# Optimization experiments

Hardware: AMD Instinct MI355X
Metric: run time of the kernel (lower is better)

Reference implementation:

```python
import jax, jax.numpy as jnp
import numpy as np

B, T, H, W, C = 32, 32, 28, 28, 1
F = 48   # conv filters
U = 8    # lstm units
EPS = 1e-3  # keras BatchNormalization default epsilon


def setup_inputs() -> dict:
    key = jax.random.key(0)
    ks = jax.random.split(key, 10)
    s = lambda fan_in: 1.0 / np.sqrt(fan_in)
    return {
        "x": jax.random.normal(ks[0], (B, T, H, W, C), jnp.float32),
        "w1": jax.random.normal(ks[1], (3, 3, C, F), jnp.float32) * s(9 * C),
        "b1": jnp.zeros((F,), jnp.float32),
        "w2": jax.random.normal(ks[2], (3, 3, F, F), jnp.float32) * s(9 * F),
        "b2": jnp.zeros((F,), jnp.float32),
        "w3": jax.random.normal(ks[3], (3, 3, F, F), jnp.float32) * s(9 * F),
        "b3": jnp.zeros((F,), jnp.float32),
        "bn1_g": jnp.ones((F,), jnp.float32),
        "bn1_b": jnp.zeros((F,), jnp.float32),
        "bn1_m": jnp.zeros((F,), jnp.float32),
        "bn1_v": jnp.ones((F,), jnp.float32),
        "wf": jax.random.normal(ks[4], (F + U, U), jnp.float32) * s(F + U),
        "bf": jnp.zeros((U,), jnp.float32),
        "wi1": jax.random.normal(ks[5], (F + U, U), jnp.float32) * s(F + U),
        "bi1": jnp.zeros((U,), jnp.float32),
        "wi2": jax.random.normal(ks[6], (F + U, U), jnp.float32) * s(F + U),
        "bi2": jnp.zeros((U,), jnp.float32),
        "wo": jax.random.normal(ks[7], (F + U, U), jnp.float32) * s(F + U),
        "bo": jnp.zeros((U,), jnp.float32),
        "bn2_g": jnp.ones((U,), jnp.float32),
        "bn2_b": jnp.zeros((U,), jnp.float32),
        "bn2_m": jnp.zeros((U,), jnp.float32),
        "bn2_v": jnp.ones((U,), jnp.float32),
        "w_out": jax.random.normal(ks[8], (U, 1), jnp.float32) * s(U),
        "b_out": jnp.zeros((1,), jnp.float32),
    }


def _conv_relu(x, w, b):
    # x: [N, H, W, Cin], w: [3, 3, Cin, Cout], SAME padding
    y = jax.lax.conv_general_dilated(
        x, w, window_strides=(1, 1), padding="SAME",
        dimension_numbers=("NHWC", "HWIO", "NHWC"))
    return jax.nn.relu(y + b)


def _bn_inf(x, g, b, m, v):
    return (x - m) * jax.lax.rsqrt(v + EPS) * g + b


def _forward(x, w1, b1, w2, b2, w3, b3, bn1_g, bn1_b, bn1_m, bn1_v,
             wf, bf, wi1, bi1, wi2, bi2, wo, bo,
             bn2_g, bn2_b, bn2_m, bn2_v, w_out, b_out):
    Bb, Tt = x.shape[0], x.shape[1]
    xf = x.reshape(Bb * Tt, H, W, C)            # fold time into batch for convs
    xf = _conv_relu(xf, w1, b1)
    xf = _conv_relu(xf, w2, b2)
    xf = _conv_relu(xf, w3, b3)
    xf = _bn_inf(xf, bn1_g, bn1_b, bn1_m, bn1_v)
    feats = xf.mean(axis=(1, 2)).reshape(Bb, Tt, F)   # GlobalAvgPool2D per frame

    def step(carry, xt):
        c, h = carry
        z = jnp.concatenate([xt, h], axis=-1)          # [B, F+U]
        f = jax.nn.sigmoid(z @ wf + bf)
        i = jax.nn.sigmoid(z @ wi1 + bi1)
        g = jnp.tanh(z @ wi2 + bi2)
        o = jax.nn.sigmoid(z @ wo + bo)
        c_new = f * c + i * g
        h_new = o * jnp.tanh(c_new)
        return (c_new, h_new), h_new

    init = (jnp.zeros((Bb, U), x.dtype), jnp.zeros((Bb, U), x.dtype))
    _, hs = jax.lax.scan(step, init, jnp.swapaxes(feats, 0, 1))  # [T, B, U]
    hs = jnp.swapaxes(hs, 0, 1)                                   # [B, T, U]
    y = _bn_inf(hs, bn2_g, bn2_b, bn2_m, bn2_v)
    return y @ w_out + b_out                                      # [B, T, 1]


def reference(x, w1, b1, w2, b2, w3, b3, bn1_g, bn1_b, bn1_m, bn1_v,
              wf, bf, wi1, bi1, wi2, bi2, wo, bo,
              bn2_g, bn2_b, bn2_m, bn2_v, w_out, b_out):
    return _forward(x, w1, b1, w2, b2, w3, b3, bn1_g, bn1_b, bn1_m, bn1_v,
                    wf, bf, wi1, bi1, wi2, bi2, wo, bo,
                    bn2_g, bn2_b, bn2_m, bn2_v, w_out, b_out)
```

## Files before the change

kernel.cpp:

```cpp
#include <hip/hip_runtime.h>
#include <stdint.h>

#define B_ 32
#define T_ 32
#define NPIX 784
#define NFRM 1024
#define EPSV 1e-3f

typedef __attribute__((ext_vector_type(8))) _Float16 half8v;
typedef __attribute__((ext_vector_type(4))) float float4v;

#define CB_STRIDE 12576
#define ZERO_OFF  75456
#define X_OFF     75472
#define W_OFF     78608
#define LDS_TOT   121616
#define WPACK     43008

__device__ __forceinline__ unsigned short f2h(float f) {
    union { _Float16 h; unsigned short u; } cv; cv.h = (_Float16)f; return cv.u;
}

__global__ __launch_bounds__(256) void pack_weights(
    const float* __restrict__ w2, const float* __restrict__ w3,
    unsigned short* __restrict__ out)
{
    int idx = blockIdx.x * 256 + threadIdx.x;
    int conv = idx / 21504;
    int r = idx - conv * 21504;
    const float* w = conv ? w3 : w2;
    int s  = r / 1536;
    int r2 = r - s * 1536;
    int q  = r2 / 384;
    int r3 = r2 - q * 384;
    int co = r3 >> 3, j = r3 & 7;
    int k  = s * 32 + q * 8 + j;
    unsigned short v = 0;
    if (k < 432) v = f2h(w[k * 48 + co]);
    out[idx] = v;
}

__device__ __forceinline__ void stage_w(char* smem, const char* g, int tid) {
    const char* gl = g + tid * 16;
    __builtin_amdgcn_global_load_lds(
        (const __attribute__((address_space(1))) unsigned int*)(gl),
        (__attribute__((address_space(3))) unsigned int*)(smem + W_OFF + tid * 16),
        16, 0, 0);
    __builtin_amdgcn_global_load_lds(
        (const __attribute__((address_space(1))) unsigned int*)(gl + 16384),
        (__attribute__((address_space(3))) unsigned int*)(smem + W_OFF + tid * 16 + 16384),
        16, 0, 0);
    if (tid < 640)
        __builtin_amdgcn_global_load_lds(
            (const __attribute__((address_space(1))) unsigned int*)(gl + 32768),
            (__attribute__((address_space(3))) unsigned int*)(smem + W_OFF + tid * 16 + 32768),
            16, 0, 0);
}

#define KLOOP                                                                  \
    _Pragma("unroll 2")                                                        \
    for (int s = 0; s < 14; ++s) {                                             \
        const char* wb = smem + W_OFF + bB + s * 3072;                         \
        half8v bv0 = *(const half8v*)(wb);                                     \
        half8v bv1 = *(const half8v*)(wb + 256);                               \
        half8v bv2 = *(const half8v*)(wb + 512);                               \
        const int k_   = s * 32 + q * 8;                                       \
        const int tap_ = (k_ * 1366) >> 16;         \
        const int kc_  = k_ - tap_ * 48;                                       \
        const int ty_  = (tap_ * 11) >> 5;            \
        const int tx_  = tap_ - ty_ * 3;                                       \
        const int aoff_ = (kc_ >> 3) * CB_STRIDE + (ty_ * 28 + tx_) * 16;      \
        _Pragma("unroll")                                                      \
        for (int mt = 0; mt < 4; ++mt) {                                       \
            if (mt < 3 || wid == 0) {                                          \
                int ad = pixb16[mt] + aoff_;                                   \
                ad = ((msks[mt] >> s) & 1) ? ad : ZERO_OFF;                    \
                half8v a = *(const half8v*)(smem + ad);                        \
                acc[mt][0] = __builtin_amdgcn_mfma_f32_16x16x32_f16(a, bv0, acc[mt][0], 0, 0, 0); \
                acc[mt][1] = __builtin_amdgcn_mfma_f32_16x16x32_f16(a, bv1, acc[mt][1], 0, 0, 0); \
                acc[mt][2] = __builtin_amdgcn_mfma_f32_16x16x32_f16(a, bv2, acc[mt][2], 0, 0, 0); \
            }                                                                  \
        }                                                                      \
    }

__global__ __launch_bounds__(1024, 1) void fused_cnn(
    const float* __restrict__ x,
    const float* __restrict__ w1, const float* __restrict__ b1,
    const float* __restrict__ b2, const float* __restrict__ b3,
    const unsigned short* __restrict__ wpack,
    float* __restrict__ feats,
    const float* __restrict__ bn_g, const float* __restrict__ bn_b,
    const float* __restrict__ bn_m, const float* __restrict__ bn_v)
{
    __shared__ __align__(16) char smem[LDS_TOT];
    const int tid = threadIdx.x;
    const int n = blockIdx.x;
    const int lane = tid & 63, wid = tid >> 6;
    const int l15 = lane & 15, q = lane >> 4;

    if (tid < 4) *(unsigned int*)(smem + ZERO_OFF + tid * 4) = 0;
    if (tid < NPIX) ((float*)(smem + X_OFF))[tid] = x[(size_t)n * NPIX + tid];
    stage_w(smem, (const char*)wpack, tid);
    __syncthreads();

    if (tid < NPIX) {
        const float* sx = (const float*)(smem + X_OFF);
        int y = tid / 28, xx = tid % 28;
        #pragma unroll
        for (int h = 0; h < 2; ++h) {
            float a[24];
            #pragma unroll
            for (int c = 0; c < 24; ++c) a[c] = b1[h * 24 + c];
            #pragma unroll
            for (int dy = 0; dy < 3; ++dy) {
                int yy = y + dy - 1;
                if ((unsigned)yy >= 28u) continue;
                #pragma unroll
                for (int dx = 0; dx < 3; ++dx) {
                    int xc = xx + dx - 1;
                    if ((unsigned)xc >= 28u) continue;
                    float xv = sx[yy * 28 + xc];
                    const float* wr = w1 + (dy * 3 + dx) * 48 + h * 24;
                    #pragma unroll
                    for (int c = 0; c < 24; ++c) a[c] += xv * wr[c];
                }
            }
            #pragma unroll
            for (int c2 = 0; c2 < 3; ++c2) {
                half8v hv;
                #pragma unroll
                for (int j = 0; j < 8; ++j)
                    hv[j] = (_Float16)fmaxf(a[c2 * 8 + j], 0.f);
                *(half8v*)(smem + (h * 3 + c2) * CB_STRIDE + tid * 16) = hv;
            }
        }
    }
    __syncthreads();

    const int bB = q * 768 + l15 * 16;

    float4v acc[4][3];
    int pixb16[4], msks[4];
    #pragma unroll
    for (int mt = 0; mt < 4; ++mt) {
        int tt = wid + mt * 16;
        int p  = tt * 16 + l15;
        int y  = (p * 9363) >> 18;
        int x2 = p - y * 28;
        pixb16[mt] = (p - 29) * 16;
        unsigned my0 = ((unsigned)(y - 1) < 28u) ? 0x007u : 0u;
        unsigned my1 = ((unsigned)(y    ) < 28u) ? 0x038u : 0u;
        unsigned my2 = ((unsigned)(y + 1) < 28u) ? 0x1C0u : 0u;
        unsigned mx0 = ((unsigned)(x2 - 1) < 28u) ? 0x049u : 0u;
        unsigned mx1 = ((unsigned)(x2    ) < 28u) ? 0x092u : 0u;
        unsigned mx2 = ((unsigned)(x2 + 1) < 28u) ? 0x124u : 0u;
        unsigned m9 = (my0 | my1 | my2) & (mx0 | mx1 | mx2);
        if (tt >= 49) m9 = 0;
        int mm = 0;
        #pragma unroll
        for (int s = 0; s < 14; ++s) {
            int k = s * 32 + q * 8;
            int tap = (k * 1366) >> 16;
            if ((m9 >> tap) & 1) mm |= (1 << s);
        }
        msks[mt] = mm;
        #pragma unroll
        for (int nt = 0; nt < 3; ++nt) {
            float bv = b2[nt * 16 + l15];
            acc[mt][nt] = (float4v){bv, bv, bv, bv};
        }
    }

    KLOOP

    __syncthreads();

    #pragma unroll
    for (int mt = 0; mt < 4; ++mt) {
        int tt = wid + mt * 16;
        if (tt >= 49) continue;
        #pragma unroll
        for (int nt = 0; nt < 3; ++nt) {
            int c = nt * 16 + l15;
            #pragma unroll
            for (int r = 0; r < 4; ++r) {
                int p = tt * 16 + q * 4 + r;
                unsigned int us = (unsigned int)f2h(fmaxf(acc[mt][nt][r], 0.f));
                unsigned int other = __shfl_xor(us, 1);
                if (!(l15 & 1)) {
                    unsigned int dw = us | (other << 16);
                    *(unsigned int*)(smem + (c >> 3) * CB_STRIDE + (c & 7) * 2 + p * 16) = dw;
                }
            }
        }
    }
    stage_w(smem, (const char*)wpack + WPACK, tid);
    __syncthreads();

    #pragma unroll
    for (int mt = 0; mt < 4; ++mt)
        #pragma unroll
        for (int nt = 0; nt < 3; ++nt) {
            float bv = b3[nt * 16 + l15];
            acc[mt][nt] = (float4v){bv, bv, bv, bv};
        }

    KLOOP

    float ps0 = 0.f, ps1 = 0.f, ps2 = 0.f;
    #pragma unroll
    for (int mt = 0; mt < 4; ++mt) {
        int tt = wid + mt * 16;
        if (tt >= 49) continue;
        #pragma unroll
        for (int r = 0; r < 4; ++r) {
            ps0 += fmaxf(acc[mt][0][r], 0.f);
            ps1 += fmaxf(acc[mt][1][r], 0.f);
            ps2 += fmaxf(acc[mt][2][r], 0.f);
        }
    }
    ps0 += __shfl_xor(ps0, 16); ps0 += __shfl_xor(ps0, 32);
    ps1 += __shfl_xor(ps1, 16); ps1 += __shfl_xor(ps1, 32);
    ps2 += __shfl_xor(ps2, 16); ps2 += __shfl_xor(ps2, 32);
    __syncthreads();
    float* sRed = (float*)smem;
    if (lane < 16) {
        sRed[wid * 48 + l15]      = ps0;
        sRed[wid * 48 + 16 + l15] = ps1;
        sRed[wid * 48 + 32 + l15] = ps2;
    }
    __syncthreads();
    if (tid < 48) {
        float s = 0.f;
        #pragma unroll
        for (int wv = 0; wv < 16; ++wv) s += sRed[wv * 48 + tid];
        float r  = rsqrtf(bn_v[tid] + EPSV);
        float sc = r * bn_g[tid] * (1.0f / 784.0f);
        float sh = bn_b[tid] - bn_m[tid] * r * bn_g[tid];
        feats[(size_t)n * 48 + tid] = s * sc + sh;
    }
}

__global__ __launch_bounds__(64) void lstm_kernel(
    const float* __restrict__ feats,
    const float* __restrict__ wf, const float* __restrict__ bfv,
    const float* __restrict__ wi1, const float* __restrict__ bi1,
    const float* __restrict__ wi2, const float* __restrict__ bi2,
    const float* __restrict__ wo, const float* __restrict__ bov,
    const float* __restrict__ g2, const float* __restrict__ b2v,
    const float* __restrict__ m2, const float* __restrict__ v2,
    const float* __restrict__ w_out, const float* __restrict__ b_out,
    float* __restrict__ out)
{
    __shared__ float sZ[56];
    __shared__ float sG[32];
    __shared__ float sS[8];
    __shared__ float sKs;

    int tid = threadIdx.x;
    int b = blockIdx.x;
    int gu = tid & 31, g = gu >> 3, u = gu & 7, half = tid >> 5;

    const float* wsrc = (g == 0) ? wf : (g == 1) ? wi1 : (g == 2) ? wi2 : wo;
    float wreg[28];
    #pragma unroll
    for (int j = 0; j < 28; ++j) wreg[j] = wsrc[(half * 28 + j) * 8 + u];
    float bias = ((g == 0) ? bfv : (g == 1) ? bi1 : (g == 2) ? bi2 : bov)[u];

    if (tid < 8) {
        float r = rsqrtf(v2[tid] + EPSV);
        sS[tid] = r * g2[tid] * w_out[tid];
        sZ[48 + tid] = 0.f;
    }
    if (tid == 0) {
        float k = b_out[0];
        for (int uu = 0; uu < 8; ++uu) {
            float r = rsqrtf(v2[uu] + EPSV);
            k += (b2v[uu] - m2[uu] * r * g2[uu]) * w_out[uu];
        }
        sKs = k;
    }

    float c = 0.f;
    const float* fb = feats + (size_t)b * T_ * 48;

    for (int t = 0; t < T_; ++t) {
        if (tid < 48) sZ[tid] = fb[t * 48 + tid];
        __syncthreads();

        float a = 0.f;
        #pragma unroll
        for (int j = 0; j < 28; ++j) a += sZ[half * 28 + j] * wreg[j];
        a += __shfl_xor(a, 32);
        a += bias;
        float v;
        if (g == 2) { float e = __expf(2.f * a); v = 1.f - 2.f / (e + 1.f); }
        else        { v = 1.f / (1.f + __expf(-a)); }
        if (tid < 32) sG[gu] = v;
        __syncthreads();

        if (tid < 8) {
            c = sG[tid] * c + sG[8 + tid] * sG[16 + tid];
            float e = __expf(2.f * c);
            float h = sG[24 + tid] * (1.f - 2.f / (e + 1.f));
            sZ[48 + tid] = h;
            float contrib = h * sS[tid];
            contrib += __shfl_xor(contrib, 1);
            contrib += __shfl_xor(contrib, 2);
            contrib += __shfl_xor(contrib, 4);
            if (tid == 0) out[b * T_ + t] = contrib + sKs;
        }
        __syncthreads();
    }
}

extern "C" void kernel_launch(void* const* d_in, const int* in_sizes, int n_in,
                              void* d_out, int out_size, void* d_ws, size_t ws_size,
                              hipStream_t stream)
{
    const float* x    = (const float*)d_in[0];
    const float* w1   = (const float*)d_in[1];
    const float* b1   = (const float*)d_in[2];
    const float* w2   = (const float*)d_in[3];
    const float* b2   = (const float*)d_in[4];
    const float* w3   = (const float*)d_in[5];
    const float* b3   = (const float*)d_in[6];
    const float* bn1g = (const float*)d_in[7];
    const float* bn1b = (const float*)d_in[8];
    const float* bn1m = (const float*)d_in[9];
    const float* bn1v = (const float*)d_in[10];
    const float* wf   = (const float*)d_in[11];
    const float* bf   = (const float*)d_in[12];
    const float* wi1  = (const float*)d_in[13];
    const float* bi1  = (const float*)d_in[14];
    const float* wi2  = (const float*)d_in[15];
    const float* bi2  = (const float*)d_in[16];
    const float* wo   = (const float*)d_in[17];
    const float* bo   = (const float*)d_in[18];
    const float* bn2g = (const float*)d_in[19];
    const float* bn2b = (const float*)d_in[20];
    const float* bn2m = (const float*)d_in[21];
    const float* bn2v = (const float*)d_in[22];
    const float* wout = (const float*)d_in[23];
    const float* bout = (const float*)d_in[24];

    unsigned short* wpack = (unsigned short*)d_ws;
    float* feats = (float*)((char*)d_ws + 2 * WPACK);
    const size_t need = 2 * WPACK + (size_t)NFRM * 48 * 4;
    if (ws_size < need) return;

    pack_weights<<<168, 256, 0, stream>>>(w2, w3, wpack);
    fused_cnn<<<NFRM, 1024, 0, stream>>>(x, w1, b1, b2, b3, wpack, feats,
                                         bn1g, bn1b, bn1m, bn1v);
    lstm_kernel<<<B_, 64, 0, stream>>>(feats, wf, bf, wi1, bi1, wi2, bi2, wo, bo,
                                       bn2g, bn2b, bn2m, bn2v, wout, bout,
                                       (float*)d_out);
}
```

Baseline: 123.7 us.

## Store conv activations in zero-padded 30x30 layout to drop boundary masking

Activations now live in a 30x30 zero-padded halo grid in LDS, so the implicit-GEMM A loads use a single base-plus-offset address with no per-tap validity mask or zero-slot select. The M dimension grows from 784 to 900 padded pixels (57 tiles instead of 49), so waves 0-8 each run a fourth tile. That adds MFMA work, and padding outputs have to be masked out of the writeback and the pooling sum. It also adds an LDS zero-fill pass and raises LDS use to about 140KB.

```diff
diff --git a/kernel.cpp b/kernel.cpp
--- a/kernel.cpp
+++ b/kernel.cpp
@@ -10,11 +10,12 @@
 typedef __attribute__((ext_vector_type(8))) _Float16 half8v;
 typedef __attribute__((ext_vector_type(4))) float float4v;
 
-#define CB_STRIDE 12576
-#define ZERO_OFF  75456
-#define X_OFF     75472
-#define W_OFF     78608
-#define LDS_TOT   121616
+#define CS        15616
+#define SLOT0     496
+#define ACT_BYTES (6 * CS)
+#define X_OFF     93696
+#define W_OFF     96832
+#define LDS_TOT   139840
 #define WPACK     43008
 
 __device__ __forceinline__ unsigned short f2h(float f) {
@@ -69,13 +70,11 @@
         const int kc_  = k_ - tap_ * 48;                                       \
         const int ty_  = (tap_ * 11) >> 5;            \
         const int tx_  = tap_ - ty_ * 3;                                       \
-        const int aoff_ = (kc_ >> 3) * CB_STRIDE + (ty_ * 28 + tx_) * 16;      \
+        const int aoff_ = (kc_ >> 3) * CS + (ty_ * 30 + tx_) * 16 - 496;       \
         _Pragma("unroll")                                                      \
         for (int mt = 0; mt < 4; ++mt) {                                       \
-            if (mt < 3 || wid == 0) {                                          \
-                int ad = pixb16[mt] + aoff_;                                   \
-                ad = ((msks[mt] >> s) & 1) ? ad : ZERO_OFF;                    \
-                half8v a = *(const half8v*)(smem + ad);                        \
+            if (mt < 3 || wid < 9) {                                           \
+                half8v a = *(const half8v*)(smem + base16[mt] + aoff_);        \
                 acc[mt][0] = __builtin_amdgcn_mfma_f32_16x16x32_f16(a, bv0, acc[mt][0], 0, 0, 0); \
                 acc[mt][1] = __builtin_amdgcn_mfma_f32_16x16x32_f16(a, bv1, acc[mt][1], 0, 0, 0); \
                 acc[mt][2] = __builtin_amdgcn_mfma_f32_16x16x32_f16(a, bv2, acc[mt][2], 0, 0, 0); \
@@ -98,14 +97,21 @@
     const int lane = tid & 63, wid = tid >> 6;
     const int l15 = lane & 15, q = lane >> 4;
 
-    if (tid < 4) *(unsigned int*)(smem + ZERO_OFF + tid * 4) = 0;
+    {
+        uint32_t* z = (uint32_t*)smem;
+        for (int i = tid; i < ACT_BYTES / 16; i += 1024) {
+            ((float4v*)smem)[i] = (float4v){0.f, 0.f, 0.f, 0.f};
+        }
+        (void)z;
+    }
     if (tid < NPIX) ((float*)(smem + X_OFF))[tid] = x[(size_t)n * NPIX + tid];
     stage_w(smem, (const char*)wpack, tid);
     __syncthreads();
 
     if (tid < NPIX) {
         const float* sx = (const float*)(smem + X_OFF);
-        int y = tid / 28, xx = tid % 28;
+        int y = tid / 28, xp = tid % 28;
+        int slot = (y + 1) * 30 + (xp + 1);
         #pragma unroll
         for (int h = 0; h < 2; ++h) {
             float a[24];
@@ -117,7 +123,7 @@
                 if ((unsigned)yy >= 28u) continue;
                 #pragma unroll
                 for (int dx = 0; dx < 3; ++dx) {
-                    int xc = xx + dx - 1;
+                    int xc = xp + dx - 1;
                     if ((unsigned)xc >= 28u) continue;
                     float xv = sx[yy * 28 + xc];
                     const float* wr = w1 + (dy * 3 + dx) * 48 + h * 24;
@@ -131,7 +137,7 @@
                 #pragma unroll
                 for (int j = 0; j < 8; ++j)
                     hv[j] = (_Float16)fmaxf(a[c2 * 8 + j], 0.f);
-                *(half8v*)(smem + (h * 3 + c2) * CB_STRIDE + tid * 16) = hv;
+                *(half8v*)(smem + (h * 3 + c2) * CS + SLOT0 + slot * 16) = hv;
             }
         }
     }
@@ -140,30 +146,23 @@
     const int bB = q * 768 + l15 * 16;
 
     float4v acc[4][3];
-    int pixb16[4], msks[4];
+    int base16[4];
+    unsigned realm[4];
     #pragma unroll
     for (int mt = 0; mt < 4; ++mt) {
         int tt = wid + mt * 16;
-        int p  = tt * 16 + l15;
-        int y  = (p * 9363) >> 18;
-        int x2 = p - y * 28;
-        pixb16[mt] = (p - 29) * 16;
-        unsigned my0 = ((unsigned)(y - 1) < 28u) ? 0x007u : 0u;
-        unsigned my1 = ((unsigned)(y    ) < 28u) ? 0x038u : 0u;
-        unsigned my2 = ((unsigned)(y + 1) < 28u) ? 0x1C0u : 0u;
-        unsigned mx0 = ((unsigned)(x2 - 1) < 28u) ? 0x049u : 0u;
-        unsigned mx1 = ((unsigned)(x2    ) < 28u) ? 0x092u : 0u;
-        unsigned mx2 = ((unsigned)(x2 + 1) < 28u) ? 0x124u : 0u;
-        unsigned m9 = (my0 | my1 | my2) & (mx0 | mx1 | mx2);
-        if (tt >= 49) m9 = 0;
-        int mm = 0;
-        #pragma unroll
-        for (int s = 0; s < 14; ++s) {
-            int k = s * 32 + q * 8;
-            int tap = (k * 1366) >> 16;
-            if ((m9 >> tap) & 1) mm |= (1 << s);
-        }
-        msks[mt] = mm;
+        base16[mt] = SLOT0 + (tt * 16 + l15) * 16;
+        int p0 = tt * 16;
+        int y0 = p0 / 30, x0 = p0 - y0 * 30;
+        unsigned rm = 0;
+        int yy = y0, xx2 = x0;
+        #pragma unroll
+        for (int jj = 0; jj < 16; ++jj) {
+            if (yy >= 1 && yy <= 28 && xx2 >= 1 && xx2 <= 28) rm |= (1u << jj);
+            ++xx2;
+            if (xx2 == 30) { xx2 = 0; ++yy; }
+        }
+        realm[mt] = rm;
         #pragma unroll
         for (int nt = 0; nt < 3; ++nt) {
             float bv = b2[nt * 16 + l15];
@@ -177,19 +176,20 @@
 
     #pragma unroll
     for (int mt = 0; mt < 4; ++mt) {
+        if (mt == 3 && wid >= 9) continue;
         int tt = wid + mt * 16;
-        if (tt >= 49) continue;
         #pragma unroll
         for (int nt = 0; nt < 3; ++nt) {
             int c = nt * 16 + l15;
             #pragma unroll
             for (int r = 0; r < 4; ++r) {
-                int p = tt * 16 + q * 4 + r;
+                int slot = tt * 16 + q * 4 + r;
                 unsigned int us = (unsigned int)f2h(fmaxf(acc[mt][nt][r], 0.f));
                 unsigned int other = __shfl_xor(us, 1);
-                if (!(l15 & 1)) {
+                if (!(l15 & 1) && ((realm[mt] >> (q * 4 + r)) & 1)) {
                     unsigned int dw = us | (other << 16);
-                    *(unsigned int*)(smem + (c >> 3) * CB_STRIDE + (c & 7) * 2 + p * 16) = dw;
+                    *(unsigned int*)(smem + (c >> 3) * CS + (c & 7) * 2
+                                     + SLOT0 + slot * 16) = dw;
                 }
             }
         }
@@ -210,13 +210,13 @@
     float ps0 = 0.f, ps1 = 0.f, ps2 = 0.f;
     #pragma unroll
     for (int mt = 0; mt < 4; ++mt) {
-        int tt = wid + mt * 16;
-        if (tt >= 49) continue;
+        if (mt == 3 && wid >= 9) continue;
         #pragma unroll
         for (int r = 0; r < 4; ++r) {
-            ps0 += fmaxf(acc[mt][0][r], 0.f);
-            ps1 += fmaxf(acc[mt][1][r], 0.f);
-            ps2 += fmaxf(acc[mt][2][r], 0.f);
+            bool rb = (realm[mt] >> (q * 4 + r)) & 1;
+            ps0 += rb ? fmaxf(acc[mt][0][r], 0.f) : 0.f;
+            ps1 += rb ? fmaxf(acc[mt][1][r], 0.f) : 0.f;
+            ps2 += rb ? fmaxf(acc[mt][2][r], 0.f) : 0.f;
         }
     }
     ps0 += __shfl_xor(ps0, 16); ps0 += __shfl_xor(ps0, 32);
```

Measured after the change: 140.5 us. 13.6% more time.

## Halve CNN block to 512 threads with seven M-tiles per wave

Applied to the files above, without the earlier changes.

The fused CNN kernel now launches 512 threads (8 waves) per frame instead of 1024. Each wave handles 7 pixel tiles instead of 4, so every B-fragment load from LDS feeds more MFMAs. The K loop is fully unrolled, and conv1 and the staging loops are reworked for the smaller block. The aim is less LDS traffic per MFMA and lower sync cost, at the price of far more accumulator registers (84 floats) and fewer waves for latency hiding.

```diff
diff --git a/kernel.cpp b/kernel.cpp
--- a/kernel.cpp
+++ b/kernel.cpp
@@ -41,24 +41,19 @@
 }
 
 __device__ __forceinline__ void stage_w(char* smem, const char* g, int tid) {
-    const char* gl = g + tid * 16;
-    __builtin_amdgcn_global_load_lds(
-        (const __attribute__((address_space(1))) unsigned int*)(gl),
-        (__attribute__((address_space(3))) unsigned int*)(smem + W_OFF + tid * 16),
-        16, 0, 0);
-    __builtin_amdgcn_global_load_lds(
-        (const __attribute__((address_space(1))) unsigned int*)(gl + 16384),
-        (__attribute__((address_space(3))) unsigned int*)(smem + W_OFF + tid * 16 + 16384),
-        16, 0, 0);
-    if (tid < 640)
-        __builtin_amdgcn_global_load_lds(
-            (const __attribute__((address_space(1))) unsigned int*)(gl + 32768),
-            (__attribute__((address_space(3))) unsigned int*)(smem + W_OFF + tid * 16 + 32768),
-            16, 0, 0);
+    #pragma unroll
+    for (int c = 0; c < 6; ++c) {
+        int idx = tid + c * 512;
+        if (idx < WPACK / 16)
+            __builtin_amdgcn_global_load_lds(
+                (const __attribute__((address_space(1))) unsigned int*)(g + idx * 16),
+                (__attribute__((address_space(3))) unsigned int*)(smem + W_OFF + idx * 16),
+                16, 0, 0);
+    }
 }
 
 #define KLOOP                                                                  \
-    _Pragma("unroll 2")                                                        \
+    _Pragma("unroll")                                                          \
     for (int s = 0; s < 14; ++s) {                                             \
         const char* wb = smem + W_OFF + bB + s * 3072;                         \
         half8v bv0 = *(const half8v*)(wb);                                     \
@@ -71,8 +66,8 @@
         const int tx_  = tap_ - ty_ * 3;                                       \
         const int aoff_ = (kc_ >> 3) * CB_STRIDE + (ty_ * 28 + tx_) * 16;      \
         _Pragma("unroll")                                                      \
-        for (int mt = 0; mt < 4; ++mt) {                                       \
-            if (mt < 3 || wid == 0) {                                          \
+        for (int mt = 0; mt < 7; ++mt) {                                       \
+            if (mt < 6 || wid == 0) {                                          \
                 int ad = pixb16[mt] + aoff_;                                   \
                 ad = ((msks[mt] >> s) & 1) ? ad : ZERO_OFF;                    \
                 half8v a = *(const half8v*)(smem + ad);                        \
@@ -83,7 +78,7 @@
         }                                                                      \
     }
 
-__global__ __launch_bounds__(1024, 1) void fused_cnn(
+__global__ __launch_bounds__(512, 1) void fused_cnn(
     const float* __restrict__ x,
     const float* __restrict__ w1, const float* __restrict__ b1,
     const float* __restrict__ b2, const float* __restrict__ b3,
@@ -99,51 +94,54 @@
     const int l15 = lane & 15, q = lane >> 4;
 
     if (tid < 4) *(unsigned int*)(smem + ZERO_OFF + tid * 4) = 0;
-    if (tid < NPIX) ((float*)(smem + X_OFF))[tid] = x[(size_t)n * NPIX + tid];
+    for (int i = tid; i < NPIX; i += 512)
+        ((float*)(smem + X_OFF))[i] = x[(size_t)n * NPIX + i];
     stage_w(smem, (const char*)wpack, tid);
     __syncthreads();
 
-    if (tid < NPIX) {
+    {
         const float* sx = (const float*)(smem + X_OFF);
-        int y = tid / 28, xx = tid % 28;
-        #pragma unroll
-        for (int h = 0; h < 2; ++h) {
-            float a[24];
-            #pragma unroll
-            for (int c = 0; c < 24; ++c) a[c] = b1[h * 24 + c];
-            #pragma unroll
-            for (int dy = 0; dy < 3; ++dy) {
-                int yy = y + dy - 1;
-                if ((unsigned)yy >= 28u) continue;
+        for (int rnd = 0; rnd < 2; ++rnd) {
+            int p = tid + rnd * 512;
+            if (p < NPIX) {
+                int y = p / 28, xx = p % 28;
+                float a[48];
                 #pragma unroll
-                for (int dx = 0; dx < 3; ++dx) {
-                    int xc = xx + dx - 1;
-                    if ((unsigned)xc >= 28u) continue;
-                    float xv = sx[yy * 28 + xc];
-                    const float* wr = w1 + (dy * 3 + dx) * 48 + h * 24;
+                for (int c = 0; c < 48; ++c) a[c] = b1[c];
+                #pragma unroll
+                for (int dy = 0; dy < 3; ++dy) {
+                    int yy = y + dy - 1;
+                    if ((unsigned)yy >= 28u) continue;
                     #pragma unroll
-                    for (int c = 0; c < 24; ++c) a[c] += xv * wr[c];
+                    for (int dx = 0; dx < 3; ++dx) {
+                        int xc = xx + dx - 1;
+                        if ((unsigned)xc >= 28u) continue;
+                        float xv = sx[yy * 28 + xc];
+                        const float* wr = w1 + (dy * 3 + dx) * 48;
+                        #pragma unroll
+                        for (int c = 0; c < 48; ++c) a[c] += xv * wr[c];
+                    }
+                }
+                #pragma unroll
+                for (int cb = 0; cb < 6; ++cb) {
+                    half8v hv;
+                    #pragma unroll
+                    for (int j = 0; j < 8; ++j)
+                        hv[j] = (_Float16)fmaxf(a[cb * 8 + j], 0.f);
+                    *(half8v*)(smem + cb * CB_STRIDE + p * 16) = hv;
                 }
             }
-            #pragma unroll
-            for (int c2 = 0; c2 < 3; ++c2) {
-                half8v hv;
-                #pragma unroll
-                for (int j = 0; j < 8; ++j)
-                    hv[j] = (_Float16)fmaxf(a[c2 * 8 + j], 0.f);
-                *(half8v*)(smem + (h * 3 + c2) * CB_STRIDE + tid * 16) = hv;
-            }
         }
     }
     __syncthreads();
 
     const int bB = q * 768 + l15 * 16;
 
-    float4v acc[4][3];
-    int pixb16[4], msks[4];
-    #pragma unroll
-    for (int mt = 0; mt < 4; ++mt) {
-        int tt = wid + mt * 16;
+    float4v acc[7][3];
+    int pixb16[7], msks[7];
+    #pragma unroll
+    for (int mt = 0; mt < 7; ++mt) {
+        int tt = wid + mt * 8;
         int p  = tt * 16 + l15;
         int y  = (p * 9363) >> 18;
         int x2 = p - y * 28;
@@ -176,8 +174,8 @@
     __syncthreads();
 
     #pragma unroll
-    for (int mt = 0; mt < 4; ++mt) {
-        int tt = wid + mt * 16;
+    for (int mt = 0; mt < 7; ++mt) {
+        int tt = wid + mt * 8;
         if (tt >= 49) continue;
         #pragma unroll
         for (int nt = 0; nt < 3; ++nt) {
@@ -198,7 +196,7 @@
     __syncthreads();
 
     #pragma unroll
-    for (int mt = 0; mt < 4; ++mt)
+    for (int mt = 0; mt < 7; ++mt)
         #pragma unroll
         for (int nt = 0; nt < 3; ++nt) {
             float bv = b3[nt * 16 + l15];
@@ -209,8 +207,8 @@
 
     float ps0 = 0.f, ps1 = 0.f, ps2 = 0.f;
     #pragma unroll
-    for (int mt = 0; mt < 4; ++mt) {
-        int tt = wid + mt * 16;
+    for (int mt = 0; mt < 7; ++mt) {
+        int tt = wid + mt * 8;
         if (tt >= 49) continue;
         #pragma unroll
         for (int r = 0; r < 4; ++r) {
@@ -233,7 +231,7 @@
     if (tid < 48) {
         float s = 0.f;
         #pragma unroll
-        for (int wv = 0; wv < 16; ++wv) s += sRed[wv * 48 + tid];
+        for (int wv = 0; wv < 8; ++wv) s += sRed[wv * 48 + tid];
         float r  = rsqrtf(bn_v[tid] + EPSV);
         float sc = r * bn_g[tid] * (1.0f / 784.0f);
         float sh = bn_b[tid] - bn_m[tid] * r * bn_g[tid];
@@ -350,8 +348,8 @@
     if (ws_size < need) return;
 
     pack_weights<<<168, 256, 0, stream>>>(w2, w3, wpack);
-    fused_cnn<<<NFRM, 1024, 0, stream>>>(x, w1, b1, b2, b3, wpack, feats,
-                                         bn1g, bn1b, bn1m, bn1v);
+    fused_cnn<<<NFRM, 512, 0, stream>>>(x, w1, b1, b2, b3, wpack, feats,
+                                        bn1g, bn1b, bn1m, bn1v);
     lstm_kernel<<<B_, 64, 0, stream>>>(feats, wf, bf, wi1, bi1, wi2, bi2, wo, bo,
                                        bn2g, bn2b, bn2m, bn2v, wout, bout,
                                        (float*)d_out);
```

Measured after the change: 126.0 us. No clear change (+1.9%).
